# Performance work log

Hardware: AMD Instinct MI355X
Metric: run time of the kernel (lower is better)

Reference implementation:

```python
import jax, jax.numpy as jnp
import numpy as np

DIM = 1024
HEADS = 16
HEAD_DIM = DIM // HEADS
B, N = 4, 4096


def setup_inputs() -> dict:
    key = jax.random.key(0)
    k1, k2, k3, k4, k5 = jax.random.split(key, 5)
    scale_in = 1.0 / np.sqrt(DIM)
    return {
        "x": jax.random.normal(k1, (B, N, DIM), dtype=jnp.float32),
        # torch nn.Linear convention: weight [out, in], y = x @ W.T + b
        "w_qkv": jax.random.uniform(k2, (3 * DIM, DIM), jnp.float32, -scale_in, scale_in),
        "b_qkv": jax.random.uniform(k3, (3 * DIM,), jnp.float32, -scale_in, scale_in),
        "w_proj": jax.random.uniform(k4, (DIM, DIM), jnp.float32, -scale_in, scale_in),
        "b_proj": jax.random.uniform(k5, (DIM,), jnp.float32, -scale_in, scale_in),
    }


def reference(x, w_qkv, b_qkv, w_proj, b_proj):
    Bx, Nx, C = x.shape
    H, D = HEADS, HEAD_DIM
    qkv = (x @ w_qkv.T + b_qkv).reshape(Bx, Nx, 3, H, D)
    q, k, v = qkv[:, :, 0], qkv[:, :, 1], qkv[:, :, 2]  # each [B, N, H, D]
    # NOTE: faithful to source — heads dim was NOT moved to batch position,
    # so attention mixes across heads per token: scores [B, N, H, H].
    scores = jnp.einsum('bnhd,bngd->bnhg', q, k) / jnp.sqrt(jnp.asarray(D, x.dtype))
    attn = jax.nn.softmax(scores, axis=-1)
    out = jnp.einsum('bnhg,bngd->bnhd', attn, v).reshape(Bx, Nx, C)
    return out @ w_proj.T + b_proj
```

## Files before the change

### kernel.cpp

```cpp
#include <hip/hip_runtime.h>
#include <hip/hip_bf16.h>
#include <stdint.h>

typedef __bf16 v8bf __attribute__((ext_vector_type(8)));
typedef float  v4f  __attribute__((ext_vector_type(4)));
typedef unsigned short u16;

#define NTOK 16384
#define KDIM 1024

__device__ __forceinline__ u16 f2bf(float f) {
  uint32_t b = __builtin_bit_cast(uint32_t, f);
  b += 0x7FFFu + ((b >> 16) & 1u);
  return (u16)(b >> 16);
}

__device__ __forceinline__ void gl_lds16(const u16* g, u16* l) {
  __builtin_amdgcn_global_load_lds(
      (const __attribute__((address_space(1))) uint32_t*)g,
      (__attribute__((address_space(3))) uint32_t*)l,
      16, 0, 0);
}

__device__ __forceinline__ void bar() {
  __builtin_amdgcn_sched_barrier(0);
  __builtin_amdgcn_s_barrier();
  __builtin_amdgcn_sched_barrier(0);
}
#define LGKM0() do { asm volatile("s_waitcnt lgkmcnt(0)" ::: "memory"); \
                     __builtin_amdgcn_sched_barrier(0); } while (0)
#define VMW(n)  do { asm volatile("s_waitcnt vmcnt(" #n ")" ::: "memory"); \
                     __builtin_amdgcn_sched_barrier(0); } while (0)

__global__ void cvt_all(const float* __restrict__ x, const float* __restrict__ wq,
                        const float* __restrict__ wp, u16* __restrict__ xo,
                        u16* __restrict__ wqo, u16* __restrict__ wpo) {
  size_t id = (size_t)blockIdx.x * 256 + threadIdx.x;
  const float* src; u16* dst;
  if (id < 2097152)      { src = x  + id * 8;              dst = xo  + id * 8; }
  else if (id < 2490368) { src = wq + (id - 2097152) * 8;  dst = wqo + (id - 2097152) * 8; }
  else                   { src = wp + (id - 2490368) * 8;  dst = wpo + (id - 2490368) * 8; }
  float4 a = *(const float4*)(src);
  float4 b = *(const float4*)(src + 4);
  union { u16 u[8]; uint4 v; } pk;
  pk.u[0]=f2bf(a.x); pk.u[1]=f2bf(a.y); pk.u[2]=f2bf(a.z); pk.u[3]=f2bf(a.w);
  pk.u[4]=f2bf(b.x); pk.u[5]=f2bf(b.y); pk.u[6]=f2bf(b.z); pk.u[7]=f2bf(b.w);
  *(uint4*)(dst) = pk.v;
}

template<int NTOT, bool OUT_BF16>
__global__ __launch_bounds__(512, 2)
void gemm_bt(const u16* __restrict__ A, const u16* __restrict__ Bw,
             const float* __restrict__ bias, void* __restrict__ out) {
  constexpr int NM = NTOK / 256;
  constexpr int NN = NTOT / 256;
  constexpr int NWG = NM * NN;
  const int bid = blockIdx.x;
  const int swz = (bid & 7) * (NWG / 8) + (bid >> 3);
  const int bm = swz % NM, bn = swz / NM;

  extern __shared__ __align__(16) u16 smem[];

  const int tid = threadIdx.x, lane = tid & 63, w = tid >> 6;
  const int wr = w >> 2, wc = w & 3;

  v4f acc[8][4];
#pragma unroll
  for (int i = 0; i < 8; ++i)
#pragma unroll
    for (int j = 0; j < 4; ++j) acc[i][j] = v4f{0.f, 0.f, 0.f, 0.f};

  const u16* Ab = A  + (size_t)bm * 256 * KDIM;
  const u16* Bb = Bw + (size_t)bn * 256 * KDIM;

  const int srow = tid >> 3;
  const int sc   = (tid & 7) ^ (srow & 7);
  const size_t soff = (size_t)srow * KDIM + (size_t)sc * 8;
  auto stageH = [&](int dstoff, const u16* src) {
    gl_lds16(src + soff, smem + dstoff + (size_t)tid * 8);
    gl_lds16(src + soff + (size_t)64 * KDIM, smem + dstoff + (size_t)tid * 8 + 4096);
  };

  const int rA  = lane & 15;
  const int ck0 = (((lane >> 4) ^ (lane & 7)) << 3);
  const int ck1 = ((((lane >> 4) + 4) ^ (lane & 7)) << 3);
  const int ha = wr * 8192;
  const int hb = 16384 + (wc >> 1) * 8192 + (wc & 1) * 64 * 64;

  v8bf Af[4][2], B0r[2][2], B1r[2][2];

#define RD_A(BUF, ROFF) do {                                                  \
  _Pragma("unroll") for (int f = 0; f < 4; ++f) {                             \
    Af[f][0] = *(const v8bf*)(smem + (BUF) + ha + ((ROFF)+f*16+rA)*64 + ck0); \
    Af[f][1] = *(const v8bf*)(smem + (BUF) + ha + ((ROFF)+f*16+rA)*64 + ck1);}\
} while (0)
#define RD_B(BUF, REG, ROFF) do {                                             \
  _Pragma("unroll") for (int g = 0; g < 2; ++g) {                             \
    REG[g][0] = *(const v8bf*)(smem + (BUF) + hb + ((ROFF)+g*16+rA)*64 + ck0);\
    REG[g][1] = *(const v8bf*)(smem + (BUF) + hb + ((ROFF)+g*16+rA)*64 + ck1);}\
} while (0)
#define MM16(FI, GI, BF) do {                                                 \
  __builtin_amdgcn_s_setprio(1);                                              \
  _Pragma("unroll") for (int f = 0; f < 4; ++f)                               \
  _Pragma("unroll") for (int g = 0; g < 2; ++g) {                             \
    acc[(FI)+f][(GI)+g] = __builtin_amdgcn_mfma_f32_16x16x32_bf16(            \
        Af[f][0], BF[g][0], acc[(FI)+f][(GI)+g], 0, 0, 0);                    \
    acc[(FI)+f][(GI)+g] = __builtin_amdgcn_mfma_f32_16x16x32_bf16(            \
        Af[f][1], BF[g][1], acc[(FI)+f][(GI)+g], 0, 0, 0);                    \
  }                                                                           \
  __builtin_amdgcn_s_setprio(0);                                              \
} while (0)

#define TILE(T, D, DN, ST, PR) do {                                           \
                                                                      \
  LGKM0(); MM16(0, 0, B0r); bar();                                            \
                                                                      \
  VMW(0);                                                                     \
  if (ST) stageH((D) + 16384, Bb + (size_t)((T)+2) * 64);                     \
  LGKM0(); MM16(0, 2, B1r);                                                   \
  RD_A((D), 64);                                                              \
  bar();                                                                      \
                                                                      \
  if (ST) stageH((D) + 24576, Bb + (size_t)128*KDIM + (size_t)((T)+2) * 64);  \
  LGKM0(); MM16(4, 2, B1r);                                                   \
  if (PR) RD_B((DN), B1r, 32);                                                \
  bar();                                                                      \
                                                                      \
  if (ST) { stageH((D) + 0,    Ab + (size_t)((T)+2) * 64);                    \
            stageH((D) + 8192, Ab + (size_t)128*KDIM + (size_t)((T)+2)*64); } \
  LGKM0(); MM16(4, 0, B0r);                                                   \
  if (PR) { RD_A((DN), 0); RD_B((DN), B0r, 0); }                              \
  bar();                                                                      \
} while (0)

  stageH(0,     Ab);
  stageH(8192,  Ab + (size_t)128 * KDIM);
  stageH(16384, Bb);
  stageH(24576, Bb + (size_t)128 * KDIM);
  stageH(32768 + 16384, Bb + 64);
  stageH(32768 + 24576, Bb + (size_t)128 * KDIM + 64);
  stageH(32768 + 0,     Ab + 64);
  stageH(32768 + 8192,  Ab + (size_t)128 * KDIM + 64);
  VMW(8);
  bar();
  RD_A(0, 0);
  RD_B(0, B0r, 0);
  RD_B(0, B1r, 32);

  for (int j = 0; j < 7; ++j) {
    TILE(2 * j,     0,     32768, 1, 1);
    TILE(2 * j + 1, 32768, 0,     1, 1);
  }
  TILE(14, 0,     32768, 0, 1);
  TILE(15, 32768, 0,     0, 0);
#undef TILE
#undef MM16
#undef RD_A
#undef RD_B

  const int col0 = bn * 256 + wc * 64 + (lane & 15);
  const int row0 = bm * 256 + wr * 128 + ((lane >> 4) << 2);
#pragma unroll
  for (int mf = 0; mf < 8; ++mf) {
#pragma unroll
    for (int nf = 0; nf < 4; ++nf) {
      const int gc = col0 + nf * 16;
      const float bv = bias[gc];
#pragma unroll
      for (int j = 0; j < 4; ++j) {
        const size_t idx = (size_t)(row0 + mf * 16 + j) * NTOT + gc;
        const float v = acc[mf][nf][j] + bv;
        if constexpr (OUT_BF16) ((u16*)out)[idx] = f2bf(v);
        else                    ((float*)out)[idx] = v;
      }
    }
  }
}

__global__ __launch_bounds__(256)
void attn_mix(const u16* __restrict__ qkv, u16* __restrict__ outp) {
  __shared__ __align__(16) u16 sq[4][3072];
  __shared__ float sp[4][16][16];
  const int tid = threadIdx.x, lane = tid & 63, w = tid >> 6;
  const size_t tok = (size_t)blockIdx.x * 4 + w;
  const u16* src = qkv + tok * 3072;
#pragma unroll
  for (int i = 0; i < 6; ++i) {
    int t = i * 64 + lane;
    int row = t >> 3;
    int c = (t & 7) ^ (row & 7);
    gl_lds16(src + row * 64 + c * 8, &sq[w][t * 8]);
  }
  __syncthreads();

  const int h = lane >> 2, gb = lane & 3;
  v8bf qv[8];
#pragma unroll
  for (int c = 0; c < 8; ++c)
    qv[c] = *(const v8bf*)&sq[w][h * 64 + ((c ^ (h & 7)) * 8)];

  float s[4];
#pragma unroll
  for (int g4 = 0; g4 < 4; ++g4) {
    const int g = gb * 4 + g4;
    float a = 0.f;
#pragma unroll
    for (int c = 0; c < 8; ++c) {
      v8bf kv = *(const v8bf*)&sq[w][1024 + g * 64 + ((c ^ (g & 7)) * 8)];
#pragma unroll
      for (int j = 0; j < 8; ++j) a += (float)qv[c][j] * (float)kv[j];
    }
    s[g4] = a * 0.125f;
  }
  float m = fmaxf(fmaxf(s[0], s[1]), fmaxf(s[2], s[3]));
  m = fmaxf(m, __shfl_xor(m, 1));
  m = fmaxf(m, __shfl_xor(m, 2));
  float p[4], sum = 0.f;
#pragma unroll
  for (int g4 = 0; g4 < 4; ++g4) { p[g4] = __expf(s[g4] - m); sum += p[g4]; }
  sum += __shfl_xor(sum, 1);
  sum += __shfl_xor(sum, 2);
  const float inv = 1.f / sum;
#pragma unroll
  for (int g4 = 0; g4 < 4; ++g4) sp[w][h][gb * 4 + g4] = p[g4] * inv;
  __syncthreads();

  float o[16];
#pragma unroll
  for (int j = 0; j < 16; ++j) o[j] = 0.f;
  const int db = gb;
#pragma unroll
  for (int g = 0; g < 16; ++g) {
    const float a = sp[w][h][g];
    v8bf v0 = *(const v8bf*)&sq[w][2048 + g * 64 + (((db * 2)     ^ (g & 7)) * 8)];
    v8bf v1 = *(const v8bf*)&sq[w][2048 + g * 64 + (((db * 2 + 1) ^ (g & 7)) * 8)];
#pragma unroll
    for (int j = 0; j < 8; ++j) { o[j] += a * (float)v0[j]; o[8 + j] += a * (float)v1[j]; }
  }
  union { u16 u[16]; uint4 v[2]; } ob;
#pragma unroll
  for (int j = 0; j < 16; ++j) ob.u[j] = f2bf(o[j]);
  u16* dst = outp + tok * 1024 + h * 64 + db * 16;
  *(uint4*)dst = ob.v[0];
  *((uint4*)dst + 1) = ob.v[1];
}

extern "C" void kernel_launch(void* const* d_in, const int* in_sizes, int n_in,
                              void* d_out, int out_size, void* d_ws, size_t ws_size,
                              hipStream_t stream) {
  const float* x      = (const float*)d_in[0];
  const float* w_qkv  = (const float*)d_in[1];
  const float* b_qkv  = (const float*)d_in[2];
  const float* w_proj = (const float*)d_in[3];
  const float* b_proj = (const float*)d_in[4];

  char* ws = (char*)d_ws;
  u16* x_bf    = (u16*)(ws);
  u16* wqkv_bf = (u16*)(ws + (size_t)33554432);
  u16* wp_bf   = (u16*)(ws + (size_t)39845888);
  u16* qkv_bf  = (u16*)(ws + (size_t)41943040);
  u16* at_bf   = (u16*)(ws + (size_t)142606336);

  (void)hipFuncSetAttribute((const void*)&gemm_bt<3072, true>,
                            hipFuncAttributeMaxDynamicSharedMemorySize, 131072);
  (void)hipFuncSetAttribute((const void*)&gemm_bt<1024, false>,
                            hipFuncAttributeMaxDynamicSharedMemorySize, 131072);

  cvt_all<<<dim3(10240), dim3(256), 0, stream>>>(x, w_qkv, w_proj,
                                                 x_bf, wqkv_bf, wp_bf);

  gemm_bt<3072, true ><<<dim3(768), dim3(512), 131072, stream>>>(x_bf, wqkv_bf, b_qkv, qkv_bf);
  attn_mix<<<dim3(4096), dim3(256), 0, stream>>>(qkv_bf, at_bf);
  gemm_bt<1024, false><<<dim3(256), dim3(512), 131072, stream>>>(at_bf, wp_bf, b_proj, d_out);
}
```

Baseline: 206.8 us.

## Make QKV GEMM persistent with prefetch of next tile during epilogue

The QKV GEMM now launches 256 workgroups, each processing three output tiles in sequence instead of one tile per workgroup. The next tile's prologue loads are issued before the current tile's epilogue stores, so global loads overlap the bias-add and write-out. Tile assignment switches to a per-XCD mapping in which each XCD owns a contiguous band of M rows, intended to improve L2 reuse. The risk is that 256 workgroups at occupancy 2 may not fill all CUs, and the persistent loop adds register pressure.

Result: faster. 199.3 us (-3.6%).

```diff
diff --git a/kernel.cpp b/kernel.cpp
--- a/kernel.cpp
+++ b/kernel.cpp
@@ -48,16 +48,13 @@
   *(uint4*)(dst) = pk.v;
 }
 
-template<int NTOT, bool OUT_BF16>
+template<int NTOT, bool OUT_BF16, int ROUNDS>
 __global__ __launch_bounds__(512, 2)
 void gemm_bt(const u16* __restrict__ A, const u16* __restrict__ Bw,
              const float* __restrict__ bias, void* __restrict__ out) {
   constexpr int NM = NTOK / 256;
-  constexpr int NN = NTOT / 256;
-  constexpr int NWG = NM * NN;
   const int bid = blockIdx.x;
-  const int swz = (bid & 7) * (NWG / 8) + (bid >> 3);
-  const int bm = swz % NM, bn = swz / NM;
+  const int xcd = bid & 7, loc = bid >> 3;
 
   extern __shared__ __align__(16) u16 smem[];
 
@@ -69,16 +66,31 @@
   for (int i = 0; i < 8; ++i)
 #pragma unroll
     for (int j = 0; j < 4; ++j) acc[i][j] = v4f{0.f, 0.f, 0.f, 0.f};
-
-  const u16* Ab = A  + (size_t)bm * 256 * KDIM;
-  const u16* Bb = Bw + (size_t)bn * 256 * KDIM;
 
   const int srow = tid >> 3;
   const int sc   = (tid & 7) ^ (srow & 7);
   const size_t soff = (size_t)srow * KDIM + (size_t)sc * 8;
+  const u16* Ab; const u16* Bb; int bm, bn;
+  auto setbase = [&](int r) {
+    int q = r * 32 + loc;
+    bm = xcd * 8 + (q & 7);
+    bn = q >> 3;
+    Ab = A  + (size_t)bm * 256 * KDIM;
+    Bb = Bw + (size_t)bn * 256 * KDIM;
+  };
   auto stageH = [&](int dstoff, const u16* src) {
     gl_lds16(src + soff, smem + dstoff + (size_t)tid * 8);
     gl_lds16(src + soff + (size_t)64 * KDIM, smem + dstoff + (size_t)tid * 8 + 4096);
+  };
+  auto prolog = [&]() {
+    stageH(0,     Ab);
+    stageH(8192,  Ab + (size_t)128 * KDIM);
+    stageH(16384, Bb);
+    stageH(24576, Bb + (size_t)128 * KDIM);
+    stageH(32768 + 16384, Bb + 64);
+    stageH(32768 + 24576, Bb + (size_t)128 * KDIM + 64);
+    stageH(32768 + 0,     Ab + 64);
+    stageH(32768 + 8192,  Ab + (size_t)128 * KDIM + 64);
   };
 
   const int rA  = lane & 15;
@@ -133,48 +145,61 @@
   bar();                                                                      \
 } while (0)
 
-  stageH(0,     Ab);
-  stageH(8192,  Ab + (size_t)128 * KDIM);
-  stageH(16384, Bb);
-  stageH(24576, Bb + (size_t)128 * KDIM);
-  stageH(32768 + 16384, Bb + 64);
-  stageH(32768 + 24576, Bb + (size_t)128 * KDIM + 64);
-  stageH(32768 + 0,     Ab + 64);
-  stageH(32768 + 8192,  Ab + (size_t)128 * KDIM + 64);
+  setbase(0);
+  prolog();
   VMW(8);
   bar();
   RD_A(0, 0);
   RD_B(0, B0r, 0);
   RD_B(0, B1r, 32);
 
-  for (int j = 0; j < 7; ++j) {
-    TILE(2 * j,     0,     32768, 1, 1);
-    TILE(2 * j + 1, 32768, 0,     1, 1);
+  for (int r = 0; r < ROUNDS; ++r) {
+    for (int j = 0; j < 7; ++j) {
+      TILE(2 * j,     0,     32768, 1, 1);
+      TILE(2 * j + 1, 32768, 0,     1, 1);
+    }
+    TILE(14, 0,     32768, 0, 1);
+    TILE(15, 32768, 0,     0, 0);
+
+    const int bmw = bm, bnw = bn;
+    if (r + 1 < ROUNDS) { setbase(r + 1); prolog(); }
+
+    {
+      const int col0 = bnw * 256 + wc * 64 + (lane & 15);
+      const int row0 = bmw * 256 + wr * 128 + ((lane >> 4) << 2);
+#pragma unroll
+      for (int mf = 0; mf < 8; ++mf) {
+#pragma unroll
+        for (int nf = 0; nf < 4; ++nf) {
+          const int gc = col0 + nf * 16;
+          const float bv = bias[gc];
+#pragma unroll
+          for (int j = 0; j < 4; ++j) {
+            const size_t idx = (size_t)(row0 + mf * 16 + j) * NTOT + gc;
+            const float v = acc[mf][nf][j] + bv;
+            if constexpr (OUT_BF16) ((u16*)out)[idx] = f2bf(v);
+            else                    ((float*)out)[idx] = v;
+          }
+        }
+      }
+    }
+
+    if (r + 1 < ROUNDS) {
+#pragma unroll
+      for (int i = 0; i < 8; ++i)
+#pragma unroll
+        for (int j = 0; j < 4; ++j) acc[i][j] = v4f{0.f, 0.f, 0.f, 0.f};
+      VMW(0);
+      bar();
+      RD_A(0, 0);
+      RD_B(0, B0r, 0);
+      RD_B(0, B1r, 32);
+    }
   }
-  TILE(14, 0,     32768, 0, 1);
-  TILE(15, 32768, 0,     0, 0);
 #undef TILE
 #undef MM16
 #undef RD_A
 #undef RD_B
-
-  const int col0 = bn * 256 + wc * 64 + (lane & 15);
-  const int row0 = bm * 256 + wr * 128 + ((lane >> 4) << 2);
-#pragma unroll
-  for (int mf = 0; mf < 8; ++mf) {
-#pragma unroll
-    for (int nf = 0; nf < 4; ++nf) {
-      const int gc = col0 + nf * 16;
-      const float bv = bias[gc];
-#pragma unroll
-      for (int j = 0; j < 4; ++j) {
-        const size_t idx = (size_t)(row0 + mf * 16 + j) * NTOT + gc;
-        const float v = acc[mf][nf][j] + bv;
-        if constexpr (OUT_BF16) ((u16*)out)[idx] = f2bf(v);
-        else                    ((float*)out)[idx] = v;
-      }
-    }
-  }
 }
 
 __global__ __launch_bounds__(256)
@@ -261,15 +286,15 @@
   u16* qkv_bf  = (u16*)(ws + (size_t)41943040);
   u16* at_bf   = (u16*)(ws + (size_t)142606336);
 
-  (void)hipFuncSetAttribute((const void*)&gemm_bt<3072, true>,
+  (void)hipFuncSetAttribute((const void*)&gemm_bt<3072, true, 3>,
                             hipFuncAttributeMaxDynamicSharedMemorySize, 131072);
-  (void)hipFuncSetAttribute((const void*)&gemm_bt<1024, false>,
+  (void)hipFuncSetAttribute((const void*)&gemm_bt<1024, false, 1>,
                             hipFuncAttributeMaxDynamicSharedMemorySize, 131072);
 
   cvt_all<<<dim3(10240), dim3(256), 0, stream>>>(x, w_qkv, w_proj,
                                                  x_bf, wqkv_bf, wp_bf);
 
-  gemm_bt<3072, true ><<<dim3(768), dim3(512), 131072, stream>>>(x_bf, wqkv_bf, b_qkv, qkv_bf);
+  gemm_bt<3072, true, 3><<<dim3(256), dim3(512), 131072, stream>>>(x_bf, wqkv_bf, b_qkv, qkv_bf);
   attn_mix<<<dim3(4096), dim3(256), 0, stream>>>(qkv_bf, at_bf);
-  gemm_bt<1024, false><<<dim3(256), dim3(512), 131072, stream>>>(at_bf, wp_bf, b_proj, d_out);
-}
+  gemm_bt<1024, false, 1><<<dim3(256), dim3(512), 131072, stream>>>(at_bf, wp_bf, b_proj, d_out);
+}
```
